# Kernel optimization log

Measured on AMD Instinct MI355X. Metric: run time of the kernel, lower is better.

## Reference

```python
import jax, jax.numpy as jnp
import numpy as np
from jax import lax

DN = ('NCHW', 'OIHW', 'NCHW')


def convbn(x, w, s, b, relu=True):
    # conv (no bias) + folded BatchNorm affine (+ optional ReLU)
    y = lax.conv_general_dilated(x, w, (1, 1), 'SAME', dimension_numbers=DN)
    y = y * s[None, :, None, None] + b[None, :, None, None]
    return jnp.maximum(y, 0.0) if relu else y


_PARAM_SHAPES = [
    ('t', (128, 256, 3, 3)), ('l', (128, 256, 3, 3)),
    ('b', (128, 256, 3, 3)), ('r', (128, 256, 3, 3)),
    ('tl3', (256, 128, 3, 3)), ('br3', (256, 128, 3, 3)),
    ('tl1', (256, 256, 1, 1)), ('br1', (256, 256, 1, 1)),
    ('tlo', (256, 256, 3, 3)), ('bro', (256, 256, 3, 3)),
]


def setup_inputs() -> dict:
    key = jax.random.key(0)
    B, C, H, W = 8, 256, 128, 128
    ks = jax.random.split(key, 3 * len(_PARAM_SHAPES) + 1)
    inp = {'x': jax.random.normal(ks[0], (B, C, H, W), jnp.float32)}
    i = 1
    for name, shape in _PARAM_SHAPES:
        cout = shape[0]
        inp['w_' + name] = jax.random.normal(ks[i], shape, jnp.float32) * 0.05
        inp['s_' + name] = 1.0 + 0.1 * jax.random.normal(ks[i + 1], (cout,), jnp.float32)
        inp['b_' + name] = 0.1 * jax.random.normal(ks[i + 2], (cout,), jnp.float32)
        i += 3
    return inp


def reference(x, w_t, s_t, b_t, w_l, s_l, b_l, w_b, s_b, b_b, w_r, s_r, b_r,
              w_tl3, s_tl3, b_tl3, w_br3, s_br3, b_br3,
              w_tl1, s_tl1, b_tl1, w_br1, s_br1, b_br1,
              w_tlo, s_tlo, b_tlo, w_bro, s_bro, b_bro):
    # directional corner pools = (reverse-)cummax along H (axis 2) or W (axis 3)
    t = convbn(x, w_t, s_t, b_t)
    tp = lax.cummax(t, axis=2, reverse=True)   # top_pool: max over rows >= h
    l = convbn(x, w_l, s_l, b_l)
    lp = lax.cummax(l, axis=3, reverse=True)   # left_pool: max over cols >= w
    bo = convbn(x, w_b, s_b, b_b)
    bp = lax.cummax(bo, axis=2)                # bottom_pool: max over rows <= h
    r = convbn(x, w_r, s_r, b_r)
    rp = lax.cummax(r, axis=3)                 # right_pool: max over cols <= w

    tl = convbn(tp + lp, w_tl3, s_tl3, b_tl3, relu=False)
    tl = jnp.maximum(tl + convbn(x, w_tl1, s_tl1, b_tl1, relu=False), 0.0)
    out_tl = convbn(tl, w_tlo, s_tlo, b_tlo)

    br = convbn(bp + rp, w_br3, s_br3, b_br3, relu=False)
    br = jnp.maximum(br + convbn(x, w_br1, s_br1, b_br1, relu=False), 0.0)
    out_br = convbn(br, w_bro, s_bro, b_bro)
    return out_tl, out_br
```

## Files before the change

kernel.cpp:

```cpp
#include <hip/hip_runtime.h>
#include <cstdint>
#include <cstddef>


typedef float  f32x4 __attribute__((ext_vector_type(4)));
typedef float  f4v   __attribute__((ext_vector_type(4)));
typedef short  s16x8 __attribute__((ext_vector_type(8)));
typedef unsigned short u16x4 __attribute__((ext_vector_type(4)));

__device__ __forceinline__ float bf2f(unsigned short u) {
    unsigned x = ((unsigned)u) << 16;
    return __builtin_bit_cast(float, x);
}
__device__ __forceinline__ unsigned short f2bf(float f) {
    unsigned u = __builtin_bit_cast(unsigned, f);
    unsigned r = (u + 0x7fffu + ((u >> 16) & 1u)) >> 16;
    return (unsigned short)r;
}

#define GL_LDS(gp, lp) __builtin_amdgcn_global_load_lds( \
    (const __attribute__((address_space(1))) unsigned int*)(const void*)(gp), \
    (__attribute__((address_space(3))) unsigned int*)(void*)(lp), 16, 0, 0)

template<int CIN, int COUT, bool RELU, bool OUTF32, bool SWZ>
__global__ __launch_bounds__(256, 4)
void conv3_mfma(const unsigned short* __restrict__ in,
                const unsigned short* __restrict__ wpk,
                const float* __restrict__ bi,
                void* __restrict__ outv)
{
    __shared__ unsigned short lds[2][8704];
    const int tid  = threadIdx.x;
    const int lane = tid & 63;
    const int wv   = tid >> 6;
    const int c    = lane & 15;
    const int g    = lane >> 4;

    constexpr int GX  = (COUT / 128) * 2;
    int gx, hy, n;
    if (SWZ) {
        constexpr int NWG = GX * 64 * 8;
        constexpr int Q   = NWG / 8;
        const int braw = blockIdx.x + GX * (blockIdx.y + 64 * blockIdx.z);
        const int wl   = (braw & 7) * Q + (braw >> 3);
        gx = wl % GX;
        const int rest = wl / GX;
        hy = rest & 63;
        n  = rest >> 6;
    } else {
        gx = blockIdx.x; hy = blockIdx.y; n = blockIdx.z;
    }
    const int wtile  = gx & 1;
    const int octile = gx >> 1;
    const int h0   = hy * 2;
    const int w0   = wtile * 64;
    const int r    = wv >> 1;
    const int ocbase = octile * 128 + (wv & 1) * 64;
    const int ocf0   = octile * 8 + (wv & 1) * 4;

    int addrB[3];
    #pragma unroll
    for (int kx = 0; kx < 3; ++kx) {
        int ps0 = c + kx;
        addrB[kx] = r * 4224 + ps0 * 64 + ((g ^ ((ps0 >> 1) & 3)) << 4);
    }

    int so[5];
    #pragma unroll
    for (int it = 0; it < 5; ++it) {
        int u   = it * 256 + tid;
        int row = u / 264;
        int rem = u - row * 264;
        int ps  = rem >> 2;
        int s   = rem & 3;
        int icq = s ^ ((ps >> 1) & 3);
        so[it] = ((n * 130 + h0 + row) * 130 + (w0 + ps)) * CIN + icq * 8;
    }

    auto STAGE = [&](int chunk, int bsel) {
        const unsigned short* bp = in + chunk * 32;
        char* lb = (char*)lds + bsel * 17408 + tid * 16;
        #pragma unroll
        for (int it = 0; it < 4; ++it)
            GL_LDS(bp + so[it], lb + it * 4096);
        if (wv == 0)
            GL_LDS(bp + so[4], lb + 16384);
    };

    f32x4 acc[4][4];
    #pragma unroll
    for (int m = 0; m < 4; ++m)
        #pragma unroll
        for (int p = 0; p < 4; ++p) acc[m][p] = 0.0f;

    const int NC = CIN / 32;
    STAGE(0, 0);
    __syncthreads();

    for (int chunk = 0; chunk < NC; ++chunk) {
        const int cur = chunk & 1;
        if (chunk + 1 < NC) STAGE(chunk + 1, cur ^ 1);
        const char* lb = (const char*)lds + cur * 17408;
        #pragma unroll
        for (int kk = 0; kk < 9; ++kk) {
            const int ky = kk / 3, kx = kk % 3;
            s16x8 af[4], bf[4];
            #pragma unroll
            for (int m = 0; m < 4; ++m)
                af[m] = *(const s16x8*)(wpk
                    + ((size_t)((chunk * 9 + kk) * (COUT / 16) + ocf0 + m)) * 512 + lane * 8);
            #pragma unroll
            for (int p = 0; p < 4; ++p)
                bf[p] = *(const s16x8*)(lb + addrB[kx] + ky * 4224 + p * 1024);
            #pragma unroll
            for (int m = 0; m < 4; ++m)
                #pragma unroll
                for (int p = 0; p < 4; ++p)
                    acc[m][p] = __builtin_amdgcn_mfma_f32_16x16x32_bf16(af[m], bf[p], acc[m][p], 0, 0, 0);
        }
        __syncthreads();
    }

    #pragma unroll
    for (int m = 0; m < 4; ++m) {
        const int oc4 = ocbase + m * 16 + g * 4;
        const f4v b4 = *(const f4v*)(bi + oc4);
        #pragma unroll
        for (int p = 0; p < 4; ++p) {
            const int w = w0 + p * 16 + c;
            float y[4];
            #pragma unroll
            for (int j = 0; j < 4; ++j) {
                y[j] = acc[m][p][j] + b4[j];
                if (RELU) y[j] = fmaxf(y[j], 0.0f);
            }
            if (OUTF32) {
                float* op = (float*)outv + (((size_t)n * COUT + oc4) << 14) + ((h0 + r) << 7) + w;
                op[0] = y[0]; op[16384] = y[1]; op[32768] = y[2]; op[49152] = y[3];
            } else {
                u16x4 pk;
                #pragma unroll
                for (int j = 0; j < 4; ++j) pk[j] = f2bf(y[j]);
                *(u16x4*)((unsigned short*)outv
                    + ((size_t)(n * 130 + h0 + r + 1) * 130 + w + 1) * COUT + oc4) = pk;
            }
        }
    }
}

__global__ __launch_bounds__(256, 4)
void conv3_tlbr(const unsigned short* __restrict__ in,
                const unsigned short* __restrict__ wq0,
                const float* __restrict__ bA,
                unsigned short* __restrict__ tt0)
{
    __shared__ unsigned short lds[2][8704];
    const int tid  = threadIdx.x;
    const int lane = tid & 63;
    const int wv   = tid >> 6;
    const int c    = lane & 15;
    const int g    = lane >> 4;

    const int b  = blockIdx.x;
    const int x  = b & 7;
    const int t  = b >> 3;
    const int q  = t & 3;
    const int ts = x + 8 * (t >> 2);
    const int wtile = ts & 1;
    const int hy    = (ts >> 1) & 63;
    const int n     = ts >> 7;
    const int h0 = hy * 2;
    const int w0 = wtile * 64;
    const int r  = wv >> 1;
    const int ocbase = (wv & 1) * 64;
    const int ocf0   = (wv & 1) * 4;

    const unsigned short* wpk = wq0 + q * 294912;
    const int outoff = ((q & 1) << 1) | (q >> 1);
    unsigned short* outv = tt0 + (size_t)outoff * ((size_t)8 * 130 * 130 * 128);
    const float* bi = bA + q * 128;

    int addrB[3];
    #pragma unroll
    for (int kx = 0; kx < 3; ++kx) {
        int ps0 = c + kx;
        addrB[kx] = r * 4224 + ps0 * 64 + ((g ^ ((ps0 >> 1) & 3)) << 4);
    }

    int so[5];
    #pragma unroll
    for (int it = 0; it < 5; ++it) {
        int u   = it * 256 + tid;
        int row = u / 264;
        int rem = u - row * 264;
        int ps  = rem >> 2;
        int s   = rem & 3;
        int icq = s ^ ((ps >> 1) & 3);
        so[it] = ((n * 130 + h0 + row) * 130 + (w0 + ps)) * 256 + icq * 8;
    }

    auto STAGE = [&](int chunk, int bsel) {
        const unsigned short* bp = in + chunk * 32;
        char* lb = (char*)lds + bsel * 17408 + tid * 16;
        #pragma unroll
        for (int it = 0; it < 4; ++it)
            GL_LDS(bp + so[it], lb + it * 4096);
        if (wv == 0)
            GL_LDS(bp + so[4], lb + 16384);
    };

    f32x4 acc[4][4];
    #pragma unroll
    for (int m = 0; m < 4; ++m)
        #pragma unroll
        for (int p = 0; p < 4; ++p) acc[m][p] = 0.0f;

    STAGE(0, 0);
    __syncthreads();

    for (int chunk = 0; chunk < 8; ++chunk) {
        const int cur = chunk & 1;
        if (chunk + 1 < 8) STAGE(chunk + 1, cur ^ 1);
        const char* lb = (const char*)lds + cur * 17408;
        #pragma unroll
        for (int kk = 0; kk < 9; ++kk) {
            const int ky = kk / 3, kx = kk % 3;
            s16x8 af[4], bf[4];
            #pragma unroll
            for (int m = 0; m < 4; ++m)
                af[m] = *(const s16x8*)(wpk
                    + ((size_t)((chunk * 9 + kk) * 8 + ocf0 + m)) * 512 + lane * 8);
            #pragma unroll
            for (int p = 0; p < 4; ++p)
                bf[p] = *(const s16x8*)(lb + addrB[kx] + ky * 4224 + p * 1024);
            #pragma unroll
            for (int m = 0; m < 4; ++m)
                #pragma unroll
                for (int p = 0; p < 4; ++p)
                    acc[m][p] = __builtin_amdgcn_mfma_f32_16x16x32_bf16(af[m], bf[p], acc[m][p], 0, 0, 0);
        }
        __syncthreads();
    }

    #pragma unroll
    for (int m = 0; m < 4; ++m) {
        const int oc4 = ocbase + m * 16 + g * 4;
        const f4v b4 = *(const f4v*)(bi + oc4);
        #pragma unroll
        for (int p = 0; p < 4; ++p) {
            const int w = w0 + p * 16 + c;
            u16x4 pk;
            #pragma unroll
            for (int j = 0; j < 4; ++j)
                pk[j] = f2bf(fmaxf(acc[m][p][j] + b4[j], 0.0f));
            *(u16x4*)(outv + ((size_t)(n * 130 + h0 + r + 1) * 130 + w + 1) * 128 + oc4) = pk;
        }
    }
}

__global__ __launch_bounds__(256, 4)
void conv3p1_k(const unsigned short* __restrict__ u0,
               const unsigned short* __restrict__ xb,
               const unsigned short* __restrict__ w30,
               const unsigned short* __restrict__ w10,
               const float* __restrict__ bsum0,
               unsigned short* __restrict__ outTL,
               unsigned short* __restrict__ outBR)
{
    __shared__ unsigned short lds[2][8704];
    const int tid  = threadIdx.x;
    const int lane = tid & 63;
    const int wv   = tid >> 6;
    const int c    = lane & 15;
    const int g    = lane >> 4;

    const int b  = blockIdx.x;
    const int x  = b & 7;
    const int s  = b >> 3;
    const int q  = s & 1;
    const int gx = (s >> 1) & 3;
    const int sp = x + 8 * (s >> 3);
    const int hy = sp & 63;
    const int n  = sp >> 6;
    const int wtile  = gx & 1;
    const int octile = gx >> 1;
    const int h0 = hy * 2;
    const int w0 = wtile * 64;
    const int r  = wv >> 1;
    const int ocbase = octile * 128 + (wv & 1) * 64;
    const int ocf0   = octile * 8 + (wv & 1) * 4;

    const unsigned short* in3 = u0 + (size_t)q * ((size_t)8 * 130 * 130 * 128);
    const unsigned short* w3  = w30 + q * 294912;
    const unsigned short* w1  = w10 + q * 65536;
    const float* bi = bsum0 + q * 256;
    unsigned short* outv = q ? outBR : outTL;

    int addrB[3];
    #pragma unroll
    for (int kx = 0; kx < 3; ++kx) {
        int ps0 = c + kx;
        addrB[kx] = r * 4224 + ps0 * 64 + ((g ^ ((ps0 >> 1) & 3)) << 4);
    }
    const int addrC1 = r * 4096 + c * 64 + ((g ^ ((c >> 1) & 3)) << 4);

    int so3[5];
    #pragma unroll
    for (int it = 0; it < 5; ++it) {
        int u   = it * 256 + tid;
        int row = u / 264;
        int rem = u - row * 264;
        int ps  = rem >> 2;
        int ss  = rem & 3;
        int icq = ss ^ ((ps >> 1) & 3);
        so3[it] = ((n * 130 + h0 + row) * 130 + (w0 + ps)) * 128 + icq * 8;
    }
    int so1[4];
    #pragma unroll
    for (int it = 0; it < 4; ++it) {
        int u   = it * 256 + tid;
        int sub = u >> 9;
        int v   = u & 511;
        int row = v >> 8;
        int rem = v & 255;
        int px  = rem >> 2;
        int ss  = rem & 3;
        int icq = ss ^ ((px >> 1) & 3);
        so1[it] = ((n * 130 + h0 + 1 + row) * 130 + (w0 + px + 1)) * 256 + sub * 32 + icq * 8;
    }

    auto STAGE3 = [&](int chunk, int bsel) {
        const unsigned short* bp = in3 + chunk * 32;
        char* lb = (char*)lds + bsel * 17408 + tid * 16;
        #pragma unroll
        for (int it = 0; it < 4; ++it)
            GL_LDS(bp + so3[it], lb + it * 4096);
        if (wv == 0)
            GL_LDS(bp + so3[4], lb + 16384);
    };
    auto STAGE1 = [&](int j, int bsel) {
        const unsigned short* bp = xb + j * 64;
        char* lb = (char*)lds + bsel * 17408 + tid * 16;
        #pragma unroll
        for (int it = 0; it < 4; ++it)
            GL_LDS(bp + so1[it], lb + it * 4096);
    };

    f32x4 acc[4][4];
    #pragma unroll
    for (int m = 0; m < 4; ++m)
        #pragma unroll
        for (int p = 0; p < 4; ++p) acc[m][p] = 0.0f;

    STAGE3(0, 0);
    __syncthreads();

    for (int ph = 0; ph < 8; ++ph) {
        const int cur = ph & 1;
        if (ph < 3)      STAGE3(ph + 1, cur ^ 1);
        else if (ph < 7) STAGE1(ph - 3, cur ^ 1);
        const char* lb = (const char*)lds + cur * 17408;
        if (ph < 4) {
            #pragma unroll
            for (int kk = 0; kk < 9; ++kk) {
                const int ky = kk / 3, kx = kk % 3;
                s16x8 af[4], bf[4];
                #pragma unroll
                for (int m = 0; m < 4; ++m)
                    af[m] = *(const s16x8*)(w3
                        + ((size_t)((ph * 9 + kk) * 16 + ocf0 + m)) * 512 + lane * 8);
                #pragma unroll
                for (int p = 0; p < 4; ++p)
                    bf[p] = *(const s16x8*)(lb + addrB[kx] + ky * 4224 + p * 1024);
                #pragma unroll
                for (int m = 0; m < 4; ++m)
                    #pragma unroll
                    for (int p = 0; p < 4; ++p)
                        acc[m][p] = __builtin_amdgcn_mfma_f32_16x16x32_bf16(af[m], bf[p], acc[m][p], 0, 0, 0);
            }
        } else {
            const int j = ph - 4;
            #pragma unroll
            for (int sub = 0; sub < 2; ++sub) {
                s16x8 af[4], bf[4];
                #pragma unroll
                for (int m = 0; m < 4; ++m)
                    af[m] = *(const s16x8*)(w1
                        + ((size_t)(((j * 2 + sub) * 16) + ocf0 + m)) * 512 + lane * 8);
                #pragma unroll
                for (int p = 0; p < 4; ++p)
                    bf[p] = *(const s16x8*)(lb + sub * 8192 + addrC1 + p * 1024);
                #pragma unroll
                for (int m = 0; m < 4; ++m)
                    #pragma unroll
                    for (int p = 0; p < 4; ++p)
                        acc[m][p] = __builtin_amdgcn_mfma_f32_16x16x32_bf16(af[m], bf[p], acc[m][p], 0, 0, 0);
            }
        }
        __syncthreads();
    }

    #pragma unroll
    for (int m = 0; m < 4; ++m) {
        const int oc4 = ocbase + m * 16 + g * 4;
        const f4v b4 = *(const f4v*)(bi + oc4);
        #pragma unroll
        for (int p = 0; p < 4; ++p) {
            const int w = w0 + p * 16 + c;
            u16x4 pk;
            #pragma unroll
            for (int j = 0; j < 4; ++j)
                pk[j] = f2bf(fmaxf(acc[m][p][j] + b4[j], 0.0f));
            *(u16x4*)(outv + ((size_t)(n * 130 + h0 + r + 1) * 130 + w + 1) * 256 + oc4) = pk;
        }
    }
}

__global__ __launch_bounds__(128)
void pool_h2_k(unsigned short* __restrict__ ta, unsigned short* __restrict__ tb)
{
    const int sel = blockIdx.x & 1;
    const int col = blockIdx.x >> 1;
    unsigned short* p = sel ? tb : ta;
    const int n = col >> 7, w = col & 127, cth = threadIdx.x;
    unsigned short* base = p + (((size_t)n * 130 + 1) * 130 + (w + 1)) * 128 + cth;
    const int stride = 130 * 128;
    float m = -3.402823466e+38f;
    if (sel == 0) {
        for (int gq = 0; gq < 16; ++gq) {
            const int h0 = 127 - gq * 8;
            float v[8];
            #pragma unroll
            for (int j = 0; j < 8; ++j) v[j] = bf2f(base[(size_t)(h0 - j) * stride]);
            unsigned short o[8];
            #pragma unroll
            for (int j = 0; j < 8; ++j) { m = fmaxf(m, v[j]); o[j] = f2bf(m); }
            #pragma unroll
            for (int j = 0; j < 8; ++j) base[(size_t)(h0 - j) * stride] = o[j];
        }
    } else {
        for (int gq = 0; gq < 16; ++gq) {
            const int h0 = gq * 8;
            float v[8];
            #pragma unroll
            for (int j = 0; j < 8; ++j) v[j] = bf2f(base[(size_t)(h0 + j) * stride]);
            unsigned short o[8];
            #pragma unroll
            for (int j = 0; j < 8; ++j) { m = fmaxf(m, v[j]); o[j] = f2bf(m); }
            #pragma unroll
            for (int j = 0; j < 8; ++j) base[(size_t)(h0 + j) * stride] = o[j];
        }
    }
}

__global__ __launch_bounds__(128)
void pool_w_add2_k(const unsigned short* __restrict__ la, unsigned short* __restrict__ ta,
                   const unsigned short* __restrict__ lb, unsigned short* __restrict__ tb)
{
    const int sel = blockIdx.x & 1;
    const int row = blockIdx.x >> 1;
    const unsigned short* ls = sel ? lb : la;
    unsigned short* td = sel ? tb : ta;
    const int n = row >> 7, hh = row & 127, cth = threadIdx.x;
    const size_t rowbase = ((size_t)(n * 130 + hh + 1) * 130) * 128 + cth;
    float m = -3.402823466e+38f;
    if (sel == 0) {
        for (int gq = 0; gq < 16; ++gq) {
            const int w0 = 127 - gq * 8;
            float lv[8], tv[8];
            #pragma unroll
            for (int j = 0; j < 8; ++j) {
                size_t off = rowbase + (size_t)(w0 - j + 1) * 128;
                lv[j] = bf2f(ls[off]); tv[j] = bf2f(td[off]);
            }
            unsigned short o[8];
            #pragma unroll
            for (int j = 0; j < 8; ++j) { m = fmaxf(m, lv[j]); o[j] = f2bf(m + tv[j]); }
            #pragma unroll
            for (int j = 0; j < 8; ++j) td[rowbase + (size_t)(w0 - j + 1) * 128] = o[j];
        }
    } else {
        for (int gq = 0; gq < 16; ++gq) {
            const int w0 = gq * 8;
            float lv[8], tv[8];
            #pragma unroll
            for (int j = 0; j < 8; ++j) {
                size_t off = rowbase + (size_t)(w0 + j + 1) * 128;
                lv[j] = bf2f(ls[off]); tv[j] = bf2f(td[off]);
            }
            unsigned short o[8];
            #pragma unroll
            for (int j = 0; j < 8; ++j) { m = fmaxf(m, lv[j]); o[j] = f2bf(m + tv[j]); }
            #pragma unroll
            for (int j = 0; j < 8; ++j) td[rowbase + (size_t)(w0 + j + 1) * 128] = o[j];
        }
    }
}

__global__ __launch_bounds__(256)
void padzero_k(unsigned short* __restrict__ t, int C)
{
    int idx = blockIdx.x * 256 + threadIdx.x;
    int n = blockIdx.y;
    int cpu = C >> 3;
    if (idx >= 516 * cpu) return;
    int cell = idx / cpu, cq = idx - cell * cpu;
    int h, w;
    if (cell < 260) { h = (cell < 130) ? -1 : 128; w = (cell % 130) - 1; }
    else { int j = cell - 260; w = (j < 128) ? -1 : 128; h = j & 127; }
    size_t off = (((size_t)n * 130 + h + 1) * 130 + (w + 1)) * C + cq * 8;
    uint4 z; z.x = 0; z.y = 0; z.z = 0; z.w = 0;
    *(uint4*)(t + off) = z;
}

__global__ __launch_bounds__(256)
void padzero_all_k(unsigned short* xb, unsigned short* tt, unsigned short* bb,
                   unsigned short* ll, unsigned short* rr, unsigned short* pbr)
{
    const int id = blockIdx.y;
    unsigned short* t = id == 0 ? xb : (id == 1 ? tt : (id == 2 ? bb :
                        (id == 3 ? ll : (id == 4 ? rr : pbr))));
    const int C = (id == 0 || id == 5) ? 256 : 128;
    int idx = blockIdx.x * 256 + threadIdx.x;
    int n = blockIdx.z;
    int cpu = C >> 3;
    if (idx >= 516 * cpu) return;
    int cell = idx / cpu, cq = idx - cell * cpu;
    int h, w;
    if (cell < 260) { h = (cell < 130) ? -1 : 128; w = (cell % 130) - 1; }
    else { int j = cell - 260; w = (j < 128) ? -1 : 128; h = j & 127; }
    size_t off = (((size_t)n * 130 + h + 1) * 130 + (w + 1)) * C + cq * 8;
    uint4 z; z.x = 0; z.y = 0; z.z = 0; z.w = 0;
    *(uint4*)(t + off) = z;
}

__global__ __launch_bounds__(256)
void transform_x_k(const float* __restrict__ x, unsigned short* __restrict__ xb)
{
    __shared__ float sm[64][132];
    const int h = blockIdx.x, n = blockIdx.y, t = threadIdx.x;
    for (int cc0 = 0; cc0 < 256; cc0 += 64) {
        __syncthreads();
        {
            int ci = t >> 7, wi = t & 127;
            #pragma unroll 8
            for (int k = 0; k < 32; ++k)
                sm[ci + 2 * k][wi] = x[((size_t)(n * 256 + cc0 + ci + 2 * k) << 14) + (h << 7) + wi];
        }
        __syncthreads();
        {
            int wi = t >> 1, cq = t & 1;
            unsigned short tmp[32];
            #pragma unroll
            for (int m2 = 0; m2 < 32; ++m2) tmp[m2] = f2bf(sm[cq * 32 + m2][wi]);
            unsigned short* dst = xb + (((size_t)n * 130 + h + 1) * 130 + wi + 1) * 256 + cc0 + cq * 32;
            #pragma unroll
            for (int q = 0; q < 4; ++q) *(uint4*)(dst + q * 8) = *(const uint4*)(tmp + q * 8);
        }
    }
}

struct PrepArgs {
    const float* w[10];
    unsigned short* dst[10];
    const float* s[10];
    const float* bv[4];
    const float* bx[4];
    float* bA; float* bsum;
};

__global__ __launch_bounds__(256)
void prepack_all_k(PrepArgs a)
{
    const int id = blockIdx.y;
    int idx = blockIdx.x * 256 + threadIdx.x;
    if (id == 10) {
        if (idx < 512) a.bA[idx] = a.bv[idx >> 7][idx & 127];
        else if (idx < 768)  { int i = idx - 512; a.bsum[i]       = a.bx[0][i] + a.bx[1][i]; }
        else if (idx < 1024) { int i = idx - 768; a.bsum[256 + i] = a.bx[2][i] + a.bx[3][i]; }
        return;
    }
    if (id >= 8) {
        if (idx >= 65536) return;
        int ic = idx & 255, oc = idx >> 8;
        float v = a.w[id][oc * 256 + ic] * a.s[id][oc];
        int chunk = ic >> 5, icr = ic & 31, gg = icr >> 3, j = icr & 7;
        int m = oc >> 4, ocr = oc & 15, ln = gg * 16 + ocr;
        a.dst[id][((size_t)(chunk * 16 + m)) * 512 + ln * 8 + j] = f2bf(v);
        return;
    }
    const int CIN  = (id < 4) ? 256 : ((id < 6) ? 128 : 256);
    const int COUT = (id < 4) ? 128 : 256;
    if (idx >= COUT * CIN * 9) return;
    int kk = idx % 9; int rest = idx / 9;
    int ic = rest % CIN; int oc = rest / CIN;
    float v = a.w[id][(size_t)(oc * CIN + ic) * 9 + kk] * a.s[id][oc];
    int chunk = ic >> 5, icr = ic & 31, gg = icr >> 3, j = icr & 7;
    int m = oc >> 4, ocr = oc & 15, ln = gg * 16 + ocr;
    a.dst[id][((size_t)((chunk * 9 + kk) * (COUT / 16) + m)) * 512 + ln * 8 + j] = f2bf(v);
}

extern "C" void kernel_launch(void* const* d_in, const int* in_sizes, int n_in,
                              void* d_out, int out_size, void* d_ws, size_t ws_size,
                              hipStream_t stream)
{
    const float* x     = (const float*)d_in[0];
    const float* w_t   = (const float*)d_in[1];
    const float* s_t   = (const float*)d_in[2];
    const float* b_t   = (const float*)d_in[3];
    const float* w_l   = (const float*)d_in[4];
    const float* s_l   = (const float*)d_in[5];
    const float* b_l   = (const float*)d_in[6];
    const float* w_b   = (const float*)d_in[7];
    const float* s_b   = (const float*)d_in[8];
    const float* b_b   = (const float*)d_in[9];
    const float* w_r   = (const float*)d_in[10];
    const float* s_r   = (const float*)d_in[11];
    const float* b_r   = (const float*)d_in[12];
    const float* w_tl3 = (const float*)d_in[13];
    const float* s_tl3 = (const float*)d_in[14];
    const float* b_tl3 = (const float*)d_in[15];
    const float* w_br3 = (const float*)d_in[16];
    const float* s_br3 = (const float*)d_in[17];
    const float* b_br3 = (const float*)d_in[18];
    const float* w_tl1 = (const float*)d_in[19];
    const float* s_tl1 = (const float*)d_in[20];
    const float* b_tl1 = (const float*)d_in[21];
    const float* w_br1 = (const float*)d_in[22];
    const float* s_br1 = (const float*)d_in[23];
    const float* b_br1 = (const float*)d_in[24];
    const float* w_tlo = (const float*)d_in[25];
    const float* s_tlo = (const float*)d_in[26];
    const float* b_tlo = (const float*)d_in[27];
    const float* w_bro = (const float*)d_in[28];
    const float* s_bro = (const float*)d_in[29];
    const float* b_bro = (const float*)d_in[30];

    typedef unsigned short ush;
    const size_t T256 = (size_t)8 * 130 * 130 * 256;
    const size_t T128 = (size_t)8 * 130 * 130 * 128;

    ush* xb = (ush*)d_ws;
    ush* tt = xb + T256;
    ush* bb = tt + T128;
    ush* ll = bb + T128;
    ush* rr = ll + T128;
    ush* wq = rr + T128;
    ush* wp_t   = wq;
    ush* wp_l   = wp_t   + 294912;
    ush* wp_b   = wp_l   + 294912;
    ush* wp_r   = wp_b   + 294912;
    ush* wp_tl3 = wp_r   + 294912;
    ush* wp_br3 = wp_tl3 + 294912;
    ush* wp_tlo = wp_br3 + 294912;
    ush* wp_bro = wp_tlo + 589824;
    ush* wp_tl1 = wp_bro + 589824;
    ush* wp_br1 = wp_tl1 + 65536;
    float* bA   = (float*)(wp_br1 + 65536);
    float* bsum = bA + 512;
    ush* tl  = ll;
    ush* pbr = (ush*)d_out;

    PrepArgs pa;
    pa.w[0] = w_t;  pa.w[1] = w_l;  pa.w[2] = w_b;  pa.w[3] = w_r;
    pa.w[4] = w_tl3; pa.w[5] = w_br3; pa.w[6] = w_tlo; pa.w[7] = w_bro;
    pa.w[8] = w_tl1; pa.w[9] = w_br1;
    pa.dst[0] = wp_t;  pa.dst[1] = wp_l;  pa.dst[2] = wp_b;  pa.dst[3] = wp_r;
    pa.dst[4] = wp_tl3; pa.dst[5] = wp_br3; pa.dst[6] = wp_tlo; pa.dst[7] = wp_bro;
    pa.dst[8] = wp_tl1; pa.dst[9] = wp_br1;
    pa.s[0] = s_t;  pa.s[1] = s_l;  pa.s[2] = s_b;  pa.s[3] = s_r;
    pa.s[4] = s_tl3; pa.s[5] = s_br3; pa.s[6] = s_tlo; pa.s[7] = s_bro;
    pa.s[8] = s_tl1; pa.s[9] = s_br1;
    pa.bv[0] = b_t; pa.bv[1] = b_l; pa.bv[2] = b_b; pa.bv[3] = b_r;
    pa.bx[0] = b_tl3; pa.bx[1] = b_tl1; pa.bx[2] = b_br3; pa.bx[3] = b_br1;
    pa.bA = bA; pa.bsum = bsum;
    prepack_all_k<<<dim3(2304, 11), dim3(256), 0, stream>>>(pa);
    padzero_all_k<<<dim3(516, 6, 8), dim3(256), 0, stream>>>(xb, tt, bb, ll, rr, pbr);
    transform_x_k<<<dim3(128, 8), dim3(256), 0, stream>>>(x, xb);

    conv3_tlbr<<<dim3(4096), dim3(256), 0, stream>>>(xb, wp_t, bA, tt);

    pool_h2_k<<<dim3(2048), dim3(128), 0, stream>>>(tt, bb);
    pool_w_add2_k<<<dim3(2048), dim3(128), 0, stream>>>(ll, tt, rr, bb);

    padzero_k<<<dim3(66, 8), dim3(256), 0, stream>>>(tl, 256);
    conv3p1_k<<<dim3(4096), dim3(256), 0, stream>>>(tt, xb, wp_tl3, wp_tl1, bsum, tl, pbr);

    conv3_mfma<256, 256, true, true, true><<<dim3(4, 64, 8), dim3(256), 0, stream>>>(
        pbr, wp_bro, b_bro, (float*)d_out + 33554432);
    conv3_mfma<256, 256, true, true, true><<<dim3(4, 64, 8), dim3(256), 0, stream>>>(
        tl, wp_tlo, b_tlo, d_out);
}
```

Baseline: 873.5 us.

## Merge final tl/br output convs into one launch with XCD-aware block mapping

Adds conv3_final, which computes both output 3x3 convs (tlo and bro) in a single 4096-block launch, remapping block IDs so consecutive blocks spread across the 8 XCDs. When the workspace is large enough, the br intermediate is moved from the output buffer into the workspace so both convs can run at the same time without overwriting their inputs. It also raises wave priority around the MFMA loop in conv3_tlbr. This is meant to remove the serialization and tail of two back-to-back launches, at the cost of extra workspace and a fallback path that depends on the workspace size.

```diff
diff --git a/kernel.cpp b/kernel.cpp
--- a/kernel.cpp
+++ b/kernel.cpp
@@ -149,6 +149,118 @@
 }
 
 __global__ __launch_bounds__(256, 4)
+void conv3_final(const unsigned short* __restrict__ tlp,
+                 const unsigned short* __restrict__ pbr,
+                 const unsigned short* __restrict__ w0,
+                 const float* __restrict__ btlo, const float* __restrict__ bbro,
+                 float* __restrict__ out)
+{
+    __shared__ unsigned short lds[2][8704];
+    const int tid  = threadIdx.x;
+    const int lane = tid & 63;
+    const int wv   = tid >> 6;
+    const int c    = lane & 15;
+    const int g    = lane >> 4;
+
+    const int braw = blockIdx.x;
+    const int wl   = (braw & 7) * 512 + (braw >> 3);
+    const int q    = wl >> 11;
+    const int v    = wl & 2047;
+    const int gx   = v & 3;
+    const int hy   = (v >> 2) & 63;
+    const int n    = v >> 8;
+    const int wtile  = gx & 1;
+    const int octile = gx >> 1;
+    const int h0 = hy * 2;
+    const int w0c = wtile * 64;
+    const int r  = wv >> 1;
+    const int ocbase = octile * 128 + (wv & 1) * 64;
+    const int ocf0   = octile * 8 + (wv & 1) * 4;
+
+    const unsigned short* in = q ? pbr : tlp;
+    const unsigned short* wpk = w0 + (size_t)q * 589824;
+    const float* bi = q ? bbro : btlo;
+    float* outv = out + (size_t)q * 33554432;
+
+    int addrB[3];
+    #pragma unroll
+    for (int kx = 0; kx < 3; ++kx) {
+        int ps0 = c + kx;
+        addrB[kx] = r * 4224 + ps0 * 64 + ((g ^ ((ps0 >> 1) & 3)) << 4);
+    }
+
+    int so[5];
+    #pragma unroll
+    for (int it = 0; it < 5; ++it) {
+        int u   = it * 256 + tid;
+        int row = u / 264;
+        int rem = u - row * 264;
+        int ps  = rem >> 2;
+        int s   = rem & 3;
+        int icq = s ^ ((ps >> 1) & 3);
+        so[it] = ((n * 130 + h0 + row) * 130 + (w0c + ps)) * 256 + icq * 8;
+    }
+
+    auto STAGE = [&](int chunk, int bsel) {
+        const unsigned short* bp = in + chunk * 32;
+        char* lb = (char*)lds + bsel * 17408 + tid * 16;
+        #pragma unroll
+        for (int it = 0; it < 4; ++it)
+            GL_LDS(bp + so[it], lb + it * 4096);
+        if (wv == 0)
+            GL_LDS(bp + so[4], lb + 16384);
+    };
+
+    f32x4 acc[4][4];
+    #pragma unroll
+    for (int m = 0; m < 4; ++m)
+        #pragma unroll
+        for (int p = 0; p < 4; ++p) acc[m][p] = 0.0f;
+
+    STAGE(0, 0);
+    __syncthreads();
+
+    for (int chunk = 0; chunk < 8; ++chunk) {
+        const int cur = chunk & 1;
+        if (chunk + 1 < 8) STAGE(chunk + 1, cur ^ 1);
+        const char* lb = (const char*)lds + cur * 17408;
+        #pragma unroll
+        for (int kk = 0; kk < 9; ++kk) {
+            const int ky = kk / 3, kx = kk % 3;
+            s16x8 af[4], bf[4];
+            #pragma unroll
+            for (int m = 0; m < 4; ++m)
+                af[m] = *(const s16x8*)(wpk
+                    + ((size_t)((chunk * 9 + kk) * 16 + ocf0 + m)) * 512 + lane * 8);
+            #pragma unroll
+            for (int p = 0; p < 4; ++p)
+                bf[p] = *(const s16x8*)(lb + addrB[kx] + ky * 4224 + p * 1024);
+            #pragma unroll
+            for (int m = 0; m < 4; ++m)
+                #pragma unroll
+                for (int p = 0; p < 4; ++p)
+                    acc[m][p] = __builtin_amdgcn_mfma_f32_16x16x32_bf16(af[m], bf[p], acc[m][p], 0, 0, 0);
+        }
+        __syncthreads();
+    }
+
+    #pragma unroll
+    for (int m = 0; m < 4; ++m) {
+        const int oc4 = ocbase + m * 16 + g * 4;
+        const f4v b4 = *(const f4v*)(bi + oc4);
+        #pragma unroll
+        for (int p = 0; p < 4; ++p) {
+            const int w = w0c + p * 16 + c;
+            float* op = outv + (((size_t)n * 256 + oc4) << 14) + ((h0 + r) << 7) + w;
+            op[0]     = fmaxf(acc[m][p][0] + b4[0], 0.0f);
+            op[16384] = fmaxf(acc[m][p][1] + b4[1], 0.0f);
+            op[32768] = fmaxf(acc[m][p][2] + b4[2], 0.0f);
+            op[49152] = fmaxf(acc[m][p][3] + b4[3], 0.0f);
+        }
+    }
+}
+
+__global__ __launch_bounds__(256, 4)
 void conv3_tlbr(const unsigned short* __restrict__ in,
                 const unsigned short* __restrict__ wq0,
                 const float* __restrict__ bA,
@@ -222,6 +334,7 @@
         const int cur = chunk & 1;
         if (chunk + 1 < 8) STAGE(chunk + 1, cur ^ 1);
         const char* lb = (const char*)lds + cur * 17408;
+        __builtin_amdgcn_s_setprio(1);
         #pragma unroll
         for (int kk = 0; kk < 9; ++kk) {
             const int ky = kk / 3, kx = kk % 3;
@@ -239,6 +352,7 @@
                 for (int p = 0; p < 4; ++p)
                     acc[m][p] = __builtin_amdgcn_mfma_f32_16x16x32_bf16(af[m], bf[p], acc[m][p], 0, 0, 0);
         }
+        __builtin_amdgcn_s_setprio(0);
         __syncthreads();
     }
 
@@ -658,8 +772,12 @@
     ush* wp_br1 = wp_tl1 + 65536;
     float* bA   = (float*)(wp_br1 + 65536);
     float* bsum = bA + 512;
+    ush* end_fixed = (ush*)(bsum + 512);
     ush* tl  = ll;
-    ush* pbr = (ush*)d_out;
+
+    const size_t used  = (size_t)(end_fixed - xb);
+    const bool roomy = ws_size >= (used + T256) * 2 + 1024;
+    ush* pbr = roomy ? end_fixed : (ush*)d_out;
 
     PrepArgs pa;
     pa.w[0] = w_t;  pa.w[1] = w_l;  pa.w[2] = w_b;  pa.w[3] = w_r;
@@ -686,8 +804,13 @@
     padzero_k<<<dim3(66, 8), dim3(256), 0, stream>>>(tl, 256);
     conv3p1_k<<<dim3(4096), dim3(256), 0, stream>>>(tt, xb, wp_tl3, wp_tl1, bsum, tl, pbr);
 
-    conv3_mfma<256, 256, true, true, true><<<dim3(4, 64, 8), dim3(256), 0, stream>>>(
-        pbr, wp_bro, b_bro, (float*)d_out + 33554432);
-    conv3_mfma<256, 256, true, true, true><<<dim3(4, 64, 8), dim3(256), 0, stream>>>(
-        tl, wp_tlo, b_tlo, d_out);
-}
+    if (roomy) {
+        conv3_final<<<dim3(4096), dim3(256), 0, stream>>>(tl, pbr, wp_tlo, b_tlo, b_bro,
+                                                          (float*)d_out);
+    } else {
+        conv3_mfma<256, 256, true, true, true><<<dim3(4, 64, 8), dim3(256), 0, stream>>>(
+            pbr, wp_bro, b_bro, (float*)d_out + 33554432);
+        conv3_mfma<256, 256, true, true, true><<<dim3(4, 64, 8), dim3(256), 0, stream>>>(
+            tl, wp_tlo, b_tlo, d_out);
+    }
+}
```

Result: slower. 975.4 us (+11.7%).
